# Performance work log

Hardware: AMD Instinct MI355X
Metric: run time of the kernel (lower is better)

## Reference

```python
import jax, jax.numpy as jnp
import numpy as np

K = 16          # top-k per pooled row
EPS = 1e-12     # tf.nn.l2_normalize epsilon


def setup_inputs() -> dict:
    key = jax.random.key(0)
    x = jax.random.normal(key, (16, 256, 128, 128), dtype=jnp.float32)
    return {"x": x}


def reference(x) -> tuple:
    # x: [B, C, H, W]; last_n_dims = 2 -> pool the trailing H*W axis.
    B, C, H, W = x.shape
    flat = x.reshape(B, C, H * W)                       # [B, C, HW]
    # tf.nn.l2_normalize(axis=-1): x / sqrt(max(sum(x^2), eps))
    sq = jnp.sum(flat * flat, axis=-1, keepdims=True)
    normed = flat * jax.lax.rsqrt(jnp.maximum(sq, EPS))  # [B, C, HW]
    top_k_value, top_k_idx = jax.lax.top_k(normed, K)    # [B, C, K]
    # decode flat indices into (h, w) coordinates (div/mod loop in original)
    h = top_k_idx // W
    w = top_k_idx % W
    coors = jnp.stack([h, w], axis=-1).astype(jnp.int32)  # [B, C, K, 2]
    return top_k_value, coors
```

## Files before the change

kernel.cpp:

```cpp
#include <hip/hip_runtime.h>


#define KSEL 16
#define HW   16384
#define WDIM 128
#define CAP  1024
#define T0   2.5f
#define NROWS 4096
#define VALS_TOTAL (NROWS * KSEL)

__global__ __launch_bounds__(256) void topk_rows(const float* __restrict__ x,
                                                 float* __restrict__ out) {
    const int row  = blockIdx.x;
    const int t    = threadIdx.x;
    const int lane = t & 63;

    __shared__ unsigned long long s_cand[CAP];
    __shared__ unsigned s_cnt;
    __shared__ float s_part[4];
    __shared__ float s_scale;

    const float4* rowp = (const float4*)(x + (size_t)row * HW);

    float4 buf[16];
    #pragma unroll
    for (int k = 0; k < 16; ++k) buf[k] = rowp[k * 256 + t];

    float sumsq = 0.0f;
    #pragma unroll
    for (int k = 0; k < 16; ++k) {
        sumsq = fmaf(buf[k].x, buf[k].x, sumsq);
        sumsq = fmaf(buf[k].y, buf[k].y, sumsq);
        sumsq = fmaf(buf[k].z, buf[k].z, sumsq);
        sumsq = fmaf(buf[k].w, buf[k].w, sumsq);
    }
    #pragma unroll
    for (int off = 32; off > 0; off >>= 1)
        sumsq += __shfl_down(sumsq, off, 64);
    if (lane == 0) s_part[t >> 6] = sumsq;
    __syncthreads();
    if (t == 0) {
        float tot = s_part[0] + s_part[1] + s_part[2] + s_part[3];
        s_scale = 1.0f / sqrtf(fmaxf(tot, 1e-12f));
    }

    float T = T0, lo = -3.0e38f, hi = 3.0e38f;
    unsigned cnt = 0;
    for (int attempt = 0; attempt < 25; ++attempt) {
        __syncthreads();
        if (t == 0) s_cnt = 0;
        __syncthreads();
        #pragma unroll
        for (int k = 0; k < 16; ++k) {
            #pragma unroll
            for (int c = 0; c < 4; ++c) {
                float v = (c == 0) ? buf[k].x : (c == 1) ? buf[k].y
                        : (c == 2) ? buf[k].z : buf[k].w;
                bool p = v > T;
                unsigned long long m = __ballot(p);
                if (m) {
                    int nb  = __popcll(m);
                    int ldr = (int)__builtin_ctzll(m);
                    unsigned base = 0;
                    if (lane == ldr) base = atomicAdd(&s_cnt, (unsigned)nb);
                    base = (unsigned)__shfl((int)base, ldr, 64);
                    if (p) {
                        unsigned pos = base +
                            (unsigned)__popcll(m & ((1ull << lane) - 1ull));
                        if (pos < CAP) {
                            unsigned u  = __float_as_uint(v);
                            unsigned mm = u ^ (((unsigned)((int)u >> 31)) | 0x80000000u);
                            int idx = k * 1024 + t * 4 + c;
                            s_cand[pos] = ((unsigned long long)mm << 32) |
                                          (unsigned)(16383 - idx);
                        }
                    }
                }
            }
        }
        __syncthreads();
        cnt = s_cnt;
        if (cnt >= KSEL && cnt <= CAP) break;
        if (cnt < KSEL) { hi = T; T = (lo < -1.0e38f) ? T - 1.0f : 0.5f * (lo + T); }
        else            { lo = T; T = (hi >  1.0e38f) ? T + 1.0f : 0.5f * (T + hi); }
    }
    if (cnt > CAP) cnt = CAP;
    const float scale = s_scale;

    for (unsigned i = t; i < cnt; i += 256) {
        unsigned long long p = s_cand[i];
        unsigned m = (unsigned)(p >> 32);
        unsigned u = (m & 0x80000000u) ? (m ^ 0x80000000u) : ~m;
        float vn = __uint_as_float(u) * scale;
        unsigned u2 = __float_as_uint(vn);
        unsigned m2 = u2 ^ (((unsigned)((int)u2 >> 31)) | 0x80000000u);
        s_cand[i] = ((unsigned long long)m2 << 32) | (p & 0xFFFFFFFFull);
    }
    __syncthreads();

    for (unsigned i = t; i < cnt; i += 256) {
        unsigned long long p = s_cand[i];
        int rank = 0;
        for (unsigned j = 0; j < cnt; ++j) rank += (s_cand[j] > p) ? 1 : 0;
        if (rank < KSEL) {
            unsigned m = (unsigned)(p >> 32);
            unsigned u = (m & 0x80000000u) ? (m ^ 0x80000000u) : ~m;
            float vn = __uint_as_float(u);
            int idx = 16383 - (int)(unsigned)(p & 0xFFFFFFFFull);
            out[row * KSEL + rank] = vn;
            float* coor = out + VALS_TOTAL + ((size_t)row * KSEL + rank) * 2;
            coor[0] = (float)(idx >> 7);
            coor[1] = (float)(idx & (WDIM - 1));
        }
    }
}

extern "C" void kernel_launch(void* const* d_in, const int* in_sizes, int n_in,
                              void* d_out, int out_size, void* d_ws, size_t ws_size,
                              hipStream_t stream) {
    const float* x = (const float*)d_in[0];
    float* out = (float*)d_out;
    topk_rows<<<NROWS, 256, 0, stream>>>(x, out);
}
```

Before: 361.3 us.

## Use 512 threads per row and per-thread atomic candidate compaction

New measurement: 391.2 us. 1.08x slower.

```diff
diff --git a/kernel.cpp b/kernel.cpp
--- a/kernel.cpp
+++ b/kernel.cpp
@@ -7,28 +7,30 @@
 #define CAP  1024
 #define T0   2.5f
 #define NROWS 4096
+#define NT   512
+#define PER  8
 #define VALS_TOTAL (NROWS * KSEL)
 
-__global__ __launch_bounds__(256) void topk_rows(const float* __restrict__ x,
-                                                 float* __restrict__ out) {
+__global__ __launch_bounds__(NT, 8) void topk_rows(const float* __restrict__ x,
+                                                   float* __restrict__ out) {
     const int row  = blockIdx.x;
     const int t    = threadIdx.x;
     const int lane = t & 63;
 
     __shared__ unsigned long long s_cand[CAP];
     __shared__ unsigned s_cnt;
-    __shared__ float s_part[4];
+    __shared__ float s_part[NT / 64];
     __shared__ float s_scale;
 
     const float4* rowp = (const float4*)(x + (size_t)row * HW);
 
-    float4 buf[16];
+    float4 buf[PER];
     #pragma unroll
-    for (int k = 0; k < 16; ++k) buf[k] = rowp[k * 256 + t];
+    for (int k = 0; k < PER; ++k) buf[k] = rowp[k * NT + t];
 
     float sumsq = 0.0f;
     #pragma unroll
-    for (int k = 0; k < 16; ++k) {
+    for (int k = 0; k < PER; ++k) {
         sumsq = fmaf(buf[k].x, buf[k].x, sumsq);
         sumsq = fmaf(buf[k].y, buf[k].y, sumsq);
         sumsq = fmaf(buf[k].z, buf[k].z, sumsq);
@@ -40,7 +42,9 @@
     if (lane == 0) s_part[t >> 6] = sumsq;
     __syncthreads();
     if (t == 0) {
-        float tot = s_part[0] + s_part[1] + s_part[2] + s_part[3];
+        float tot = 0.0f;
+        #pragma unroll
+        for (int i = 0; i < NT / 64; ++i) tot += s_part[i];
         s_scale = 1.0f / sqrtf(fmaxf(tot, 1e-12f));
     }
 
@@ -50,30 +54,33 @@
         __syncthreads();
         if (t == 0) s_cnt = 0;
         __syncthreads();
+
+        unsigned msk = 0;
         #pragma unroll
-        for (int k = 0; k < 16; ++k) {
+        for (int k = 0; k < PER; ++k) {
+            msk |= (buf[k].x > T) ? (1u << (4 * k + 0)) : 0u;
+            msk |= (buf[k].y > T) ? (1u << (4 * k + 1)) : 0u;
+            msk |= (buf[k].z > T) ? (1u << (4 * k + 2)) : 0u;
+            msk |= (buf[k].w > T) ? (1u << (4 * k + 3)) : 0u;
+        }
+        unsigned base = 0;
+        if (msk) base = atomicAdd(&s_cnt, (unsigned)__popc(msk));
+        if (msk) {
             #pragma unroll
-            for (int c = 0; c < 4; ++c) {
-                float v = (c == 0) ? buf[k].x : (c == 1) ? buf[k].y
-                        : (c == 2) ? buf[k].z : buf[k].w;
-                bool p = v > T;
-                unsigned long long m = __ballot(p);
-                if (m) {
-                    int nb  = __popcll(m);
-                    int ldr = (int)__builtin_ctzll(m);
-                    unsigned base = 0;
-                    if (lane == ldr) base = atomicAdd(&s_cnt, (unsigned)nb);
-                    base = (unsigned)__shfl((int)base, ldr, 64);
-                    if (p) {
-                        unsigned pos = base +
-                            (unsigned)__popcll(m & ((1ull << lane) - 1ull));
-                        if (pos < CAP) {
+            for (int k = 0; k < PER; ++k) {
+                #pragma unroll
+                for (int c = 0; c < 4; ++c) {
+                    float v = (c == 0) ? buf[k].x : (c == 1) ? buf[k].y
+                            : (c == 2) ? buf[k].z : buf[k].w;
+                    if (v > T) {
+                        if (base < CAP) {
                             unsigned u  = __float_as_uint(v);
                             unsigned mm = u ^ (((unsigned)((int)u >> 31)) | 0x80000000u);
-                            int idx = k * 1024 + t * 4 + c;
-                            s_cand[pos] = ((unsigned long long)mm << 32) |
-                                          (unsigned)(16383 - idx);
+                            int idx = (k * NT + t) * 4 + c;
+                            s_cand[base] = ((unsigned long long)mm << 32) |
+                                           (unsigned)(16383 - idx);
                         }
+                        base++;
                     }
                 }
             }
@@ -87,7 +94,7 @@
     if (cnt > CAP) cnt = CAP;
     const float scale = s_scale;
 
-    for (unsigned i = t; i < cnt; i += 256) {
+    for (unsigned i = t; i < cnt; i += NT) {
         unsigned long long p = s_cand[i];
         unsigned m = (unsigned)(p >> 32);
         unsigned u = (m & 0x80000000u) ? (m ^ 0x80000000u) : ~m;
@@ -98,7 +105,7 @@
     }
     __syncthreads();
 
-    for (unsigned i = t; i < cnt; i += 256) {
+    for (unsigned i = t; i < cnt; i += NT) {
         unsigned long long p = s_cand[i];
         int rank = 0;
         for (unsigned j = 0; j < cnt; ++j) rank += (s_cand[j] > p) ? 1 : 0;
@@ -120,5 +127,5 @@
                               hipStream_t stream) {
     const float* x = (const float*)d_in[0];
     float* out = (float*)d_out;
-    topk_rows<<<NROWS, 256, 0, stream>>>(x, out);
+    topk_rows<<<NROWS, NT, 0, stream>>>(x, out);
 }
```
